# Optimization experiments

Hardware: AMD Instinct MI355X
Metric: run time of the kernel (lower is better)

The kernel has to match this reference:

```python
import jax, jax.numpy as jnp
import numpy as np

P_DROP = 0.2
NEG_SLOPE = 0.2


def setup_inputs() -> dict:
    key = jax.random.key(0)
    ks = jax.random.split(key, 12)
    N, E = 50000, 800000
    IN, H1, H2, OUT = 256, 256, 128, 64
    x = jax.random.normal(ks[0], (N, IN), dtype=jnp.float32)
    adj_rows = jax.random.randint(ks[1], (E,), 0, N, dtype=jnp.int32)
    adj_cols = jax.random.randint(ks[2], (E,), 0, N, dtype=jnp.int32)
    adj_vals = jax.random.uniform(ks[3], (E,), dtype=jnp.float32)
    W1 = jax.random.normal(ks[4], (H1, IN), dtype=jnp.float32) * (1.0 / np.sqrt(IN))
    b1 = jax.random.normal(ks[5], (H1,), dtype=jnp.float32) * 0.01
    W2 = jax.random.normal(ks[6], (H2, H1), dtype=jnp.float32) * (1.0 / np.sqrt(H1))
    b2 = jax.random.normal(ks[7], (H2,), dtype=jnp.float32) * 0.01
    W3 = jax.random.normal(ks[8], (OUT, H2), dtype=jnp.float32) * (1.0 / np.sqrt(H2))
    b3 = jax.random.normal(ks[9], (OUT,), dtype=jnp.float32) * 0.01
    mask1 = jax.random.bernoulli(ks[10], 1.0 - P_DROP, (N, H1))
    mask2 = jax.random.bernoulli(ks[11], 1.0 - P_DROP, (N, H2))
    return {"x": x, "adj_rows": adj_rows, "adj_cols": adj_cols, "adj_vals": adj_vals,
            "W1": W1, "b1": b1, "W2": W2, "b2": b2, "W3": W3, "b3": b3,
            "mask1": mask1, "mask2": mask2}


def _spmm(rows, cols, vals, h, n_nodes):
    # sparse adjacency matmul: out[r] = sum_e vals[e] * h[cols[e]] for rows[e]==r
    msgs = vals[:, None] * h[cols]  # [E, d] irregular gather
    return jax.ops.segment_sum(msgs, rows, num_segments=n_nodes)


def _gcn_layer(x, W, b, rows, cols, vals, n_nodes):
    h = x @ W.T + b  # nn.Linear
    return _spmm(rows, cols, vals, h, n_nodes)


def reference(x, adj_rows, adj_cols, adj_vals, W1, b1, W2, b2, W3, b3, mask1, mask2):
    N = x.shape[0]
    keep = 1.0 / (1.0 - P_DROP)
    h = _gcn_layer(x, W1, b1, adj_rows, adj_cols, adj_vals, N)
    h = jnp.where(h >= 0, h, NEG_SLOPE * h)
    h = jnp.where(mask1, h * keep, 0.0)
    h = _gcn_layer(h, W2, b2, adj_rows, adj_cols, adj_vals, N)
    h = jnp.where(h >= 0, h, NEG_SLOPE * h)
    h = jnp.where(mask2, h * keep, 0.0)
    z = _gcn_layer(h, W3, b3, adj_rows, adj_cols, adj_vals, N)
    return z
```

## Files before the change

kernel.cpp:

```cpp
#include <hip/hip_runtime.h>


typedef unsigned short ushort_t;
typedef __attribute__((ext_vector_type(8))) short bf16x8;
typedef __attribute__((ext_vector_type(4))) float f32x4;
typedef __attribute__((ext_vector_type(2))) unsigned int u32x2;
typedef __attribute__((ext_vector_type(4))) unsigned int u32x4;

__device__ __forceinline__ float bf2f(ushort_t u) {
  return __uint_as_float(((unsigned int)u) << 16);
}
__device__ __forceinline__ ushort_t f2bf(float f) {
  unsigned int u = __float_as_uint(f);
  return (ushort_t)((u + 0x7FFFu + ((u >> 16) & 1u)) >> 16);
}
__device__ __forceinline__ float read_f(const void* p, int fm, size_t i) {
  return fm ? bf2f(((const ushort_t*)p)[i]) : ((const float*)p)[i];
}

__device__ __forceinline__ size_t frag_off(int m, int k, int K) {
  return (size_t)(m >> 4) * 16 * K + ((size_t)(k >> 5) << 9) +
         (((k >> 3) & 3) << 7) + ((m & 15) << 3) + (k & 7);
}

__global__ void prep_kernel(const void* __restrict__ x,
                            const void* __restrict__ m1,
                            const void* __restrict__ m2,
                            int* __restrict__ modes,
                            int* __restrict__ zero_region, int zn,
                            const void* __restrict__ W1, const void* __restrict__ W2,
                            const void* __restrict__ W3,
                            const void* __restrict__ b1, const void* __restrict__ b2,
                            const void* __restrict__ b3,
                            ushort_t* __restrict__ whi, ushort_t* __restrict__ wlo,
                            float* __restrict__ biasf,
                            int n1, int n2, int n3, int h1, int h2, int h3,
                            int K1, int K2, int K3) {
  if (blockIdx.x == 0) {
    __shared__ int bfok;
    if (threadIdx.x == 0) bfok = 1;
    __syncthreads();
    for (int i = threadIdx.x; i < 8192; i += blockDim.x) {
      ushort_t h = ((const ushort_t*)x)[i];
      int e = (h >> 7) & 0xFF;
      if (!(h == 0 || (e >= 95 && e <= 133))) atomicAnd(&bfok, 0);
    }
    __syncthreads();
    if (threadIdx.x == 0) modes[0] = bfok;
  } else if (blockIdx.x <= 2) {
    const void* p = (blockIdx.x == 1) ? m1 : m2;
    __shared__ int ok[4];
    if (threadIdx.x < 4) ok[threadIdx.x] = 1;
    __syncthreads();
    for (int i = threadIdx.x; i < 4096; i += blockDim.x) {
      unsigned int w = ((const unsigned int*)p)[i];
      if (!(w == 0u || w == 1u)) atomicAnd(&ok[0], 0);
      if (!(w == 0u || w == 0x3F800000u)) atomicAnd(&ok[1], 0);
      unsigned int h16 = w >> 16, l16 = w & 0xFFFFu;
      if (!((h16 == 0u || h16 == 0x3F80u) && (l16 == 0u || l16 == 0x3F80u)))
        atomicAnd(&ok[2], 0);
      if (((w | (w >> 8) | (w >> 16) | (w >> 24)) & 0xFEu) != 0u) atomicAnd(&ok[3], 0);
    }
    __syncthreads();
    if (threadIdx.x == 0)
      modes[blockIdx.x] = ok[0] ? 1 : (ok[1] ? 2 : (ok[2] ? 3 : 0));
  } else if (blockIdx.x < 35) {
    __shared__ int bfok;
    if (threadIdx.x == 0) bfok = 1;
    __syncthreads();
    for (int i = threadIdx.x; i < 8192; i += blockDim.x) {
      ushort_t h = ((const ushort_t*)x)[i];
      int e = (h >> 7) & 0xFF;
      if (!(h == 0 || (e >= 95 && e <= 133))) atomicAnd(&bfok, 0);
    }
    __syncthreads();
    int fm = bfok;
    int wtot = n1 + n2 + n3;
    int total = wtot + h1 + h2 + h3;
    for (int i = (blockIdx.x - 3) * 256 + threadIdx.x; i < total; i += 32 * 256) {
      if (i < wtot) {
        const void* src; int j, K; size_t base;
        if (i < n1) { src = W1; j = i; K = K1; base = 0; }
        else if (i < n1 + n2) { src = W2; j = i - n1; K = K2; base = n1; }
        else { src = W3; j = i - n1 - n2; K = K3; base = (size_t)n1 + n2; }
        int n = j / K, k = j - n * K;
        float v = read_f(src, fm, j);
        ushort_t h = f2bf(v);
        size_t o = base + frag_off(n, k, K);
        whi[o] = h;
        wlo[o] = f2bf(v - bf2f(h));
      } else {
        int k = i - wtot;
        const void* src; int j;
        if (k < h1) { src = b1; j = k; }
        else if (k < h1 + h2) { src = b2; j = k - h1; }
        else { src = b3; j = k - h1 - h2; }
        biasf[k] = read_f(src, fm, j);
      }
    }
  } else {
    int i = (blockIdx.x - 35) * blockDim.x + threadIdx.x;
    int stride = (gridDim.x - 35) * blockDim.x;
    for (; i < zn; i += stride) zero_region[i] = 0;
  }
}

__global__ void hist_bin_kernel(
    const int* __restrict__ rows, const int* __restrict__ cols,
    const void* __restrict__ vals, const int* __restrict__ fm_p,
    int* __restrict__ h8, int* __restrict__ cnt_ovf, int* __restrict__ binfill,
    int2* __restrict__ bins, int cap, int use_bins, int4* __restrict__ ovf,
    int E, int Nrows, const void* __restrict__ x, ushort_t* __restrict__ xbf,
    int K1, int nx) {
  int fm = *fm_p;
  const int BIN_BLOCKS = 1024;
  if (blockIdx.x < BIN_BLOCKS) {
    int xcd = blockIdx.x & 7;
    if (use_bins) {
      __shared__ int hist[8];
      __shared__ int gbase[8];
      __shared__ int pfx[8];
      __shared__ int2 stage[1024];
      int tid = threadIdx.x;
      for (int tb = blockIdx.x; tb * 1024 < E; tb += BIN_BLOCKS) {
        int base = tb * 1024;
        if (tid < 8) hist[tid] = 0;
        __syncthreads();
        int rr[4], cc[4], pp[4], rk[4]; float vv[4];
#pragma unroll
        for (int j = 0; j < 4; ++j) {
          int i = base + j * 256 + tid;
          if (i < E) {
            rr[j] = rows[i]; cc[j] = cols[i]; vv[j] = read_f(vals, fm, i);
            pp[j] = rr[j] >> 13;
            rk[j] = atomicAdd(&hist[pp[j]], 1);
          } else {
            pp[j] = -1;
          }
        }
        __syncthreads();
        if (tid == 0) {
          int s = 0;
#pragma unroll
          for (int q = 0; q < 8; ++q) { pfx[q] = s; s += hist[q]; }
        }
        if (tid < 8)
          gbase[tid] = atomicAdd(&binfill[(xcd << 4) + tid], hist[tid]);
        __syncthreads();
#pragma unroll
        for (int j = 0; j < 4; ++j) {
          if (pp[j] >= 0)
            stage[pfx[pp[j]] + rk[j]] =
                make_int2((rr[j] << 16) | cc[j], __float_as_int(vv[j]));
        }
        __syncthreads();
        int total = pfx[7] + hist[7];
        for (int k = tid; k < total; k += 256) {
          int p = 0;
#pragma unroll
          for (int q = 1; q < 8; ++q) p += (k >= pfx[q]);
          int2 ent = stage[k];
          int pos = gbase[p] + (k - pfx[p]);
          if (pos < cap) {
            bins[(size_t)((xcd << 3) + p) * cap + pos] = ent;
          } else {
            int r = ((unsigned int)ent.x) >> 16;
            int orank = atomicAdd(&cnt_ovf[r], 1);
            int op = atomicAdd(&binfill[128], 1);
            ovf[op] = make_int4(r, ent.x & 0xFFFF, ent.y, orank);
          }
        }
        __syncthreads();
      }
    } else {
      int* cnt_s = h8 + (size_t)xcd * Nrows;
      int i = blockIdx.x * blockDim.x + threadIdx.x;
      int stride = BIN_BLOCKS * blockDim.x;
      for (; i < E; i += stride) atomicAdd(&cnt_s[rows[i]], 1);
    }
  } else {
    if (fm == 1) return;
    int nx4 = nx / 4;
    int i = (blockIdx.x - BIN_BLOCKS) * blockDim.x + threadIdx.x;
    int stride = (gridDim.x - BIN_BLOCKS) * blockDim.x;
    for (; i < nx4; i += stride) {
      int m = i / (K1 / 4);
      int k0 = (i - m * (K1 / 4)) * 4;
      f32x4 v = ((const f32x4*)x)[i];
      ushort_t p0 = f2bf(v[0]), p1 = f2bf(v[1]), p2 = f2bf(v[2]), p3 = f2bf(v[3]);
      size_t o = frag_off(m, k0, K1);
      *(u32x2*)(xbf + o) = (u32x2){
          (unsigned int)p0 | ((unsigned int)p1 << 16),
          (unsigned int)p2 | ((unsigned int)p3 << 16)};
    }
  }
}

__global__ __launch_bounds__(256) void count_kernel(
    const int2* __restrict__ bins, const int* __restrict__ binfill,
    int cap, int* __restrict__ h8, int Nrows, int use_bins) {
  if (!use_bins) return;
  int x = blockIdx.x >> 3, p = blockIdx.x & 7;
  __shared__ int hist[8192];
  for (int i = threadIdx.x; i < 8192; i += 256) hist[i] = 0;
  __syncthreads();
  int n = binfill[x * 16 + p];
  if (n > cap) n = cap;
  const int2* bp = bins + (size_t)((x << 3) + p) * cap;
  for (int e = threadIdx.x; e < n; e += 256) {
    int r = ((unsigned int)bp[e].x) >> 16;
    atomicAdd(&hist[r & 8191], 1);
  }
  __syncthreads();
  int r0 = p << 13;
  for (int i = threadIdx.x; i < 8192; i += 256) {
    int r = r0 + i;
    if (r < Nrows) h8[(size_t)x * Nrows + r] = hist[i];
  }
}

__global__ __launch_bounds__(256) void scan_fused_kernel(
    const int* __restrict__ h8, const int* __restrict__ cnt_ovf,
    int* __restrict__ pub, int* __restrict__ row_start,
    int* __restrict__ sb8, int n) {
  int b = blockIdx.x, t = threadIdx.x;
  int i = b * 256 + t;
  int hx[8];
  int v = 0, ov = 0;
  if (i < n) {
#pragma unroll
    for (int x = 0; x < 8; ++x) { hx[x] = h8[(size_t)x * n + i]; v += hx[x]; }
    ov = cnt_ovf[i];
  } else {
#pragma unroll
    for (int x = 0; x < 8; ++x) hx[x] = 0;
  }
  int vt = v + ov;
  __shared__ int s[256];
  s[t] = vt;
  __syncthreads();
  for (int off = 1; off < 256; off <<= 1) {
    int a_ = s[t];
    int y_ = (t >= off) ? s[t - off] : 0;
    __syncthreads();
    s[t] = a_ + y_;
    __syncthreads();
  }
  int incl = s[t];
  int total = s[255];
  if (t == 0)
    __hip_atomic_store(&pub[b], (total << 1) | 1, __ATOMIC_RELEASE,
                       __HIP_MEMORY_SCOPE_AGENT);
  int contrib = 0;
  for (int t0 = t; t0 < b; t0 += 256) {
    int p;
    do {
      p = __hip_atomic_load(&pub[t0], __ATOMIC_ACQUIRE,
                            __HIP_MEMORY_SCOPE_AGENT);
    } while (!(p & 1));
    contrib += (p >> 1);
  }
  __syncthreads();
  s[t] = contrib;
  __syncthreads();
  for (int off = 128; off > 0; off >>= 1) {
    if (t < off) s[t] += s[t + off];
    __syncthreads();
  }
  int base = s[0];
  int rs = base + incl - vt;
  if (i < n) {
    row_start[i] = rs;
    int acc = rs;
#pragma unroll
    for (int x = 0; x < 8; ++x) { sb8[(size_t)x * n + i] = acc; acc += hx[x]; }
    sb8[(size_t)8 * n + i] = acc;
  }
  if (i == n - 1) row_start[n] = base + incl;
}

template<int KC>
__device__ __forceinline__ void load_afrag(const ushort_t* __restrict__ A,
                                           const ushort_t* __restrict__ Xrow,
                                           bool rowA, int mtile, int K,
                                           int lane, int mr, int quad, int M,
                                           bf16x8* dst) {
  if (rowA) {
    int rr = mtile * 16 + mr;
    if (rr >= M) rr = M - 1;
    const ushort_t* ap = Xrow + (size_t)rr * K + quad * 8;
#pragma unroll
    for (int kc = 0; kc < KC; ++kc) dst[kc] = *(const bf16x8*)(ap + kc * 32);
  } else {
    const ushort_t* ap = A + (size_t)mtile * 16 * K + lane * 8;
#pragma unroll
    for (int kc = 0; kc < KC; ++kc) dst[kc] = *(const bf16x8*)(ap + kc * 512);
  }
}

template<int KC>
__device__ __forceinline__ void gemm_dev(
    int vbid, int nblk, int tid,
    const ushort_t* __restrict__ A, const ushort_t* __restrict__ Xrow, int fm,
    const ushort_t* __restrict__ Whi, const ushort_t* __restrict__ Wlo,
    const float* __restrict__ bias, ushort_t* __restrict__ g, int ldg,
    int M, int nct) {
  const int K = KC * 32;
  int wave = tid >> 6, lane = tid & 63;
  int gw = vbid * 4 + wave;
  int NW = nblk * 4;
  int mr = lane & 15, quad = lane >> 4;
  int ct = gw % nct;
  int nrt = (M + 15) >> 4;
  int ntasks = nct * nrt;
  if (gw >= ntasks) return;

  bool rowA = (Xrow != nullptr) && (fm != 0);

  bf16x8 wh[KC], wl[KC];
  {
    const ushort_t* wp = Whi + (size_t)ct * 16 * K + lane * 8;
    const ushort_t* wq = Wlo + (size_t)ct * 16 * K + lane * 8;
#pragma unroll
    for (int kc = 0; kc < KC; ++kc) {
      wh[kc] = *(const bf16x8*)(wp + kc * 512);
      wl[kc] = *(const bf16x8*)(wq + kc * 512);
    }
  }
  int col = ct * 16 + mr;
  float bv = bias[col];

  int task = gw;
  bf16x8 af[KC];
  load_afrag<KC>(A, Xrow, rowA, task / nct, K, lane, mr, quad, M, af);

#pragma unroll 1
  for (;;) {
    int next = task + NW;
    bool has_next = next < ntasks;
    bf16x8 afn[KC];
    if (has_next)
      load_afrag<KC>(A, Xrow, rowA, next / nct, K, lane, mr, quad, M, afn);

    f32x4 acc[4];
#pragma unroll
    for (int t = 0; t < 4; ++t) acc[t] = (f32x4){0.f, 0.f, 0.f, 0.f};
#pragma unroll
    for (int kc = 0; kc < KC; ++kc) {
      acc[(2 * kc) & 3] = __builtin_amdgcn_mfma_f32_16x16x32_bf16(af[kc], wh[kc], acc[(2 * kc) & 3], 0, 0, 0);
      acc[(2 * kc + 1) & 3] = __builtin_amdgcn_mfma_f32_16x16x32_bf16(af[kc], wl[kc], acc[(2 * kc + 1) & 3], 0, 0, 0);
    }
    int m0 = (task / nct) * 16;
#pragma unroll
    for (int r = 0; r < 4; ++r) {
      int row = m0 + quad * 4 + r;
      float s = ((acc[0][r] + acc[1][r]) + (acc[2][r] + acc[3][r])) + bv;
      if (row < M) g[(size_t)row * ldg + col] = f2bf(s);
    }
    if (!has_next) break;
#pragma unroll
    for (int kc = 0; kc < KC; ++kc) af[kc] = afn[kc];
    task = next;
  }
}

template<int KC>
__global__ __launch_bounds__(256) void gemm_breg_kernel(
    const ushort_t* __restrict__ A,
    const ushort_t* __restrict__ Xrow, const int* __restrict__ fm_p,
    const ushort_t* __restrict__ Whi, const ushort_t* __restrict__ Wlo,
    const float* __restrict__ bias, ushort_t* __restrict__ g, int ldg,
    int M, int nct) {
  gemm_dev<KC>(blockIdx.x, gridDim.x, threadIdx.x, A, Xrow, *fm_p,
               Whi, Wlo, bias, g, ldg, M, nct);
}

__global__ __launch_bounds__(256) void scatter_gemm_kernel(
    const int2* __restrict__ bins, const int* __restrict__ binfill,
    const int* __restrict__ row_start, int* __restrict__ fill,
    const int* __restrict__ sb8, int Nrows,
    int2* __restrict__ ecv, int cap, const int4* __restrict__ ovf,
    const int* __restrict__ rows, const int* __restrict__ cols,
    const void* __restrict__ vals, const int* __restrict__ fm_p,
    int use_bins, int E,
    const ushort_t* __restrict__ A, const ushort_t* __restrict__ Xrow,
    const ushort_t* __restrict__ Whi, const ushort_t* __restrict__ Wlo,
    const float* __restrict__ bias, ushort_t* __restrict__ g, int ldg,
    int M, int nct) {
  __shared__ int sbl[8192];
  if (blockIdx.x >= 64) {
    gemm_dev<8>(blockIdx.x - 64, 1024, threadIdx.x, A, Xrow, *fm_p,
                Whi, Wlo, bias, g, ldg, M, nct);
    return;
  }
  if (use_bins) {
    int x = blockIdx.x >> 3, p = blockIdx.x & 7;
    int r0 = p << 13;
    for (int i = threadIdx.x; i < 8192; i += 256) {
      int r = r0 + i;
      sbl[i] = (r < Nrows) ? sb8[(size_t)x * Nrows + r] : 0;
    }
    __syncthreads();
    int n = binfill[x * 16 + p];
    if (n > cap) n = cap;
    const int2* bp = bins + (size_t)((x << 3) + p) * cap;
    for (int e = threadIdx.x; e < n; e += 256) {
      int2 ent = bp[e];
      int r = ((unsigned int)ent.x) >> 16;
      int pos = atomicAdd(&sbl[r & 8191], 1);
      ecv[pos] = make_int2(ent.x & 0xFFFF, ent.y);
    }
    int ovfn = binfill[128];
    for (int e = blockIdx.x * 256 + (int)threadIdx.x; e < ovfn; e += 64 * 256) {
      int4 t = ovf[e];
      ecv[sb8[(size_t)8 * Nrows + t.x] + t.w] = make_int2(t.y, t.z);
    }
  } else {
    int fm = *fm_p;
    for (int i = blockIdx.x * 256 + (int)threadIdx.x; i < E; i += 64 * 256) {
      int r = rows[i];
      int pos = atomicAdd(&fill[r], 1);
      ecv[row_start[r] + pos] = make_int2(cols[i], __float_as_int(read_f(vals, fm, i)));
    }
  }
}

template<int VEC, int CHUNK, bool CLAMP>
__device__ __forceinline__ void spmm_chunk(const int2* __restrict__ ecv,
                                           int base, int e1,
                                           const ushort_t* __restrict__ G,
                                           int D, int f0, float* a) {
  int2 cv[CHUNK];
#pragma unroll
  for (int j = 0; j < CHUNK; ++j) {
    int ee = base + j;
    if (CLAMP) ee = (ee < e1) ? ee : e1 - 1;
    cv[j] = ecv[ee];
  }
  float v[CHUNK];
#pragma unroll
  for (int j = 0; j < CHUNK; ++j) {
    v[j] = __int_as_float(cv[j].y);
    if (CLAMP && (base + j >= e1)) v[j] = 0.f;
  }
  if (VEC == 4) {
    u32x2 gg[CHUNK];
#pragma unroll
    for (int j = 0; j < CHUNK; ++j)
      gg[j] = *(const u32x2*)(G + (size_t)cv[j].x * D + f0);
#pragma unroll
    for (int j = 0; j < CHUNK; ++j) {
      a[0] += v[j] * bf2f((ushort_t)gg[j][0]);
      a[1] += v[j] * bf2f((ushort_t)(gg[j][0] >> 16));
      a[2] += v[j] * bf2f((ushort_t)gg[j][1]);
      a[3] += v[j] * bf2f((ushort_t)(gg[j][1] >> 16));
    }
  } else if (VEC == 2) {
    unsigned int gg[CHUNK];
#pragma unroll
    for (int j = 0; j < CHUNK; ++j)
      gg[j] = *(const unsigned int*)(G + (size_t)cv[j].x * D + f0);
#pragma unroll
    for (int j = 0; j < CHUNK; ++j) {
      a[0] += v[j] * bf2f((ushort_t)gg[j]);
      a[1] += v[j] * bf2f((ushort_t)(gg[j] >> 16));
    }
  } else {
    ushort_t h[CHUNK];
#pragma unroll
    for (int j = 0; j < CHUNK; ++j) h[j] = G[(size_t)cv[j].x * D + f0];
#pragma unroll
    for (int j = 0; j < CHUNK; ++j) a[0] += v[j] * bf2f(h[j]);
  }
}

template<int MODE, int VEC>
__global__ __launch_bounds__(256) void spmm8_kernel(
    const int* __restrict__ row_start, const int2* __restrict__ ecv,
    const ushort_t* __restrict__ G, int D,
    const void* __restrict__ mask, const int* __restrict__ mmode_p,
    void* __restrict__ outp, int N) {
  __shared__ ushort_t stage[1024];
  int wave = threadIdx.x >> 6, lane = threadIdx.x & 63;
  int r = blockIdx.x * 4 + wave;
  bool active = r < N;
  float a[VEC];
#pragma unroll
  for (int q = 0; q < VEC; ++q) a[q] = 0.f;
  int f0 = lane * VEC;

  bool keep[VEC];
#pragma unroll
  for (int q = 0; q < VEC; ++q) keep[q] = true;
  if (MODE == 1 && active) {
    size_t om = (size_t)r * D + f0;
    int mm = *mmode_p;
    if (mm == 1 || mm == 2) {
      if (VEC == 4) {
        u32x4 mv = *(const u32x4*)((const unsigned int*)mask + om);
#pragma unroll
        for (int q = 0; q < VEC; ++q) keep[q] = mv[q] != 0u;
      } else if (VEC == 2) {
        u32x2 mv = *(const u32x2*)((const unsigned int*)mask + om);
#pragma unroll
        for (int q = 0; q < VEC; ++q) keep[q] = mv[q] != 0u;
      } else {
        keep[0] = ((const unsigned int*)mask)[om] != 0u;
      }
    } else if (mm == 3) {
      if (VEC == 4) {
        u32x2 mv = *(const u32x2*)((const ushort_t*)mask + om);
        keep[0] = (mv[0] & 0xFFFFu) != 0u; keep[1] = (mv[0] >> 16) != 0u;
        keep[2] = (mv[1] & 0xFFFFu) != 0u; keep[3] = (mv[1] >> 16) != 0u;
      } else if (VEC == 2) {
        unsigned int mv = *(const unsigned int*)((const ushort_t*)mask + om);
        keep[0] = (mv & 0xFFFFu) != 0u; keep[1] = (mv >> 16) != 0u;
      } else {
        keep[0] = ((const ushort_t*)mask)[om] != 0;
      }
    } else {
      if (VEC == 4) {
        unsigned int mv = *(const unsigned int*)((const unsigned char*)mask + om);
        keep[0] = (mv & 0xFFu) != 0u;         keep[1] = ((mv >> 8) & 0xFFu) != 0u;
        keep[2] = ((mv >> 16) & 0xFFu) != 0u; keep[3] = (mv >> 24) != 0u;
      } else if (VEC == 2) {
        unsigned int mv = *(const unsigned short*)((const unsigned char*)mask + om);
        keep[0] = (mv & 0xFFu) != 0u; keep[1] = ((mv >> 8) & 0xFFu) != 0u;
      } else {
        keep[0] = ((const unsigned char*)mask)[om] != 0;
      }
    }
  }

  if (active) {
    int e  = __builtin_amdgcn_readfirstlane(row_start[r]);
    int e1 = __builtin_amdgcn_readfirstlane(row_start[r + 1]);
    for (; e + 16 <= e1; e += 16)
      spmm_chunk<VEC, 16, false>(ecv, e, e1, G, D, f0, a);
    for (; e < e1; e += 8)
      spmm_chunk<VEC, 8, true>(ecv, e, e1, G, D, f0, a);
  }

  if (MODE == 1) {
    if (active) {
#pragma unroll
      for (int q = 0; q < VEC; ++q) {
        float t = a[q];
        t = (t >= 0.f) ? t : 0.2f * t;
        t = keep[q] ? t * 1.25f : 0.f;
        stage[wave * D + f0 + q] = f2bf(t);
      }
    }
    __syncthreads();
    if (threadIdx.x < D) {
      int g = threadIdx.x >> 3, s = threadIdx.x & 7;
      int kc = g >> 2, quad = g & 3;
      int sr = s >> 1;
      int r0 = blockIdx.x * 4;
      if (r0 + sr < N) {
        int kk = kc * 32 + quad * 8 + (s & 1) * 4;
        size_t dst = (size_t)(r0 >> 4) * 16 * D + ((size_t)kc << 9) +
                     (quad << 7) + ((r0 & 15) << 3) + s * 4;
        *(u32x2*)((ushort_t*)outp + dst) = *(const u32x2*)(stage + sr * D + kk);
      }
    }
  } else {
    if (active) {
      size_t o = (size_t)r * D + f0;
#pragma unroll
      for (int q = 0; q < VEC; ++q) ((float*)outp)[o + q] = a[q];
    }
  }
}

extern "C" void kernel_launch(void* const* d_in, const int* in_sizes, int n_in,
                              void* d_out, int out_size, void* d_ws, size_t ws_size,
                              hipStream_t stream) {
  const void* x     = d_in[0];
  const int*  rows  = (const int*)d_in[1];
  const int*  cols  = (const int*)d_in[2];
  const void* vals  = d_in[3];
  const void* W1    = d_in[4];
  const void* b1    = d_in[5];
  const void* W2    = d_in[6];
  const void* b2    = d_in[7];
  const void* W3    = d_in[8];
  const void* b3    = d_in[9];
  const void* mask1 = d_in[10];
  const void* mask2 = d_in[11];

  const int H1  = in_sizes[5];
  const int H2  = in_sizes[7];
  const int OUT = in_sizes[9];
  const int IN  = in_sizes[4] / H1;
  const int N   = in_sizes[0] / IN;
  const int E   = in_sizes[1];
  const int W1n = in_sizes[4], W2n = in_sizes[6], W3n = in_sizes[8];
  const int Np  = ((N + 15) / 16) * 16;
  const int CAP = (E >> 5) + 2048;
  const int use_bins = (N <= 65535) ? 1 : 0;
  const int P = (N + 255) / 256;

  char* ws = (char*)d_ws;
  size_t off = 0;
  auto alloc = [&](size_t bytes) -> void* {
    void* p = ws + off;
    off = (off + bytes + 255) & ~(size_t)255;
    return p;
  };
  int*      modes     = (int*)alloc(4 * 4);
  int*      row_start = (int*)alloc((size_t)(N + 1) * 4);
  int*      meta      = (int*)alloc(((size_t)10 * N + 512) * 4);
  int*      sb8       = (int*)alloc((size_t)9 * N * 4);
  int2*     ecv       = (int2*)alloc((size_t)E * 8);
  int2*     bins      = (int2*)alloc((size_t)64 * CAP * 8);
  int4*     ovf       = (int4*)alloc((size_t)E * 16);
  ushort_t* whi       = (ushort_t*)alloc((size_t)(W1n + W2n + W3n) * 2);
  ushort_t* wlo       = (ushort_t*)alloc((size_t)(W1n + W2n + W3n) * 2);
  float*    biasf     = (float*)alloc((size_t)(H1 + H2 + OUT) * 4);
  ushort_t* bufA      = (ushort_t*)alloc((size_t)Np * H1 * 2);
  ushort_t* bufB      = (ushort_t*)alloc((size_t)Np * H1 * 2);
  ushort_t* bufC      = (ushort_t*)bins;

  int* fmode   = modes;
  int* mm1     = modes + 1;
  int* mm2     = modes + 2;
  int* h8      = meta;
  int* cnt_ovf = meta + 8 * N;
  int* fill    = meta + 9 * N;
  int* binfill = meta + 10 * N;
  int* pub     = meta + 10 * N + 256;
  ushort_t* w1hi = whi,             *w1lo = wlo;
  ushort_t* w2hi = whi + W1n,       *w2lo = wlo + W1n;
  ushort_t* w3hi = whi + W1n + W2n, *w3lo = wlo + W1n + W2n;

  prep_kernel<<<512, 256, 0, stream>>>(
      x, mask1, mask2, modes, meta, 10 * N + 512,
      W1, W2, W3, b1, b2, b3, whi, wlo, biasf,
      W1n, W2n, W3n, H1, H2, OUT, IN, H1, H2);

  hist_bin_kernel<<<2048, 256, 0, stream>>>(
      rows, cols, vals, fmode, h8, cnt_ovf, binfill, bins, CAP, use_bins, ovf,
      E, N, x, bufA, IN, N * IN);

  count_kernel<<<64, 256, 0, stream>>>(bins, binfill, CAP, h8, N, use_bins);

  scan_fused_kernel<<<P, 256, 0, stream>>>(h8, cnt_ovf, pub, row_start, sb8, N);

  scatter_gemm_kernel<<<1088, 256, 0, stream>>>(
      bins, binfill, row_start, fill, sb8, N, ecv, CAP, ovf,
      rows, cols, vals, fmode, use_bins, E,
      bufA, (const ushort_t*)x, w1hi, w1lo, biasf, bufB, H1, N, H1 / 16);

  int spmm_grid = (N + 3) / 4;
  const int GEMM_BLOCKS = 1024;

  spmm8_kernel<1, 4><<<spmm_grid, 256, 0, stream>>>(
      row_start, ecv, bufB, H1, mask1, mm1, bufC, N);
  gemm_breg_kernel<8><<<GEMM_BLOCKS, 256, 0, stream>>>(
      bufC, nullptr, fmode, w2hi, w2lo, biasf + H1, bufB, H2, N, H2 / 16);
  spmm8_kernel<1, 2><<<spmm_grid, 256, 0, stream>>>(
      row_start, ecv, bufB, H2, mask2, mm2, bufA, N);
  gemm_breg_kernel<4><<<GEMM_BLOCKS, 256, 0, stream>>>(
      bufA, nullptr, fmode, w3hi, w3lo, biasf + H1 + H2, bufB, OUT, N, OUT / 16);
  spmm8_kernel<0, 1><<<spmm_grid, 256, 0, stream>>>(
      row_start, ecv, bufB, OUT, nullptr, fmode, d_out, N);
}
```

Baseline: 406.7 us.

## Store GEMM outputs in 32-column panels and run SpMM per panel

```diff
diff --git a/kernel.cpp b/kernel.cpp
--- a/kernel.cpp
+++ b/kernel.cpp
@@ -303,7 +303,7 @@
     int vbid, int nblk, int tid,
     const ushort_t* __restrict__ A, const ushort_t* __restrict__ Xrow, int fm,
     const ushort_t* __restrict__ Whi, const ushort_t* __restrict__ Wlo,
-    const float* __restrict__ bias, ushort_t* __restrict__ g, int ldg,
+    const float* __restrict__ bias, ushort_t* __restrict__ g, int Np,
     int M, int nct) {
   const int K = KC * 32;
   int wave = tid >> 6, lane = tid & 63;
@@ -329,6 +329,7 @@
   }
   int col = ct * 16 + mr;
   float bv = bias[col];
+  ushort_t* gp = g + (size_t)(col >> 5) * Np * 32 + (col & 31);
 
   int task = gw;
   bf16x8 af[KC];
@@ -355,7 +356,7 @@
     for (int r = 0; r < 4; ++r) {
       int row = m0 + quad * 4 + r;
       float s = ((acc[0][r] + acc[1][r]) + (acc[2][r] + acc[3][r])) + bv;
-      if (row < M) g[(size_t)row * ldg + col] = f2bf(s);
+      if (row < M) gp[(size_t)row * 32] = f2bf(s);
     }
     if (!has_next) break;
 #pragma unroll
@@ -369,10 +370,10 @@
     const ushort_t* __restrict__ A,
     const ushort_t* __restrict__ Xrow, const int* __restrict__ fm_p,
     const ushort_t* __restrict__ Whi, const ushort_t* __restrict__ Wlo,
-    const float* __restrict__ bias, ushort_t* __restrict__ g, int ldg,
+    const float* __restrict__ bias, ushort_t* __restrict__ g, int Np,
     int M, int nct) {
   gemm_dev<KC>(blockIdx.x, gridDim.x, threadIdx.x, A, Xrow, *fm_p,
-               Whi, Wlo, bias, g, ldg, M, nct);
+               Whi, Wlo, bias, g, Np, M, nct);
 }
 
 __global__ __launch_bounds__(256) void scatter_gemm_kernel(
@@ -385,12 +386,12 @@
     int use_bins, int E,
     const ushort_t* __restrict__ A, const ushort_t* __restrict__ Xrow,
     const ushort_t* __restrict__ Whi, const ushort_t* __restrict__ Wlo,
-    const float* __restrict__ bias, ushort_t* __restrict__ g, int ldg,
+    const float* __restrict__ bias, ushort_t* __restrict__ g, int Np,
     int M, int nct) {
   __shared__ int sbl[8192];
   if (blockIdx.x >= 64) {
     gemm_dev<8>(blockIdx.x - 64, 1024, threadIdx.x, A, Xrow, *fm_p,
-                Whi, Wlo, bias, g, ldg, M, nct);
+                Whi, Wlo, bias, g, Np, M, nct);
     return;
   }
   if (use_bins) {
@@ -425,151 +426,79 @@
   }
 }
 
-template<int VEC, int CHUNK, bool CLAMP>
-__device__ __forceinline__ void spmm_chunk(const int2* __restrict__ ecv,
-                                           int base, int e1,
-                                           const ushort_t* __restrict__ G,
-                                           int D, int f0, float* a) {
-  int2 cv[CHUNK];
-#pragma unroll
-  for (int j = 0; j < CHUNK; ++j) {
-    int ee = base + j;
-    if (CLAMP) ee = (ee < e1) ? ee : e1 - 1;
-    cv[j] = ecv[ee];
-  }
-  float v[CHUNK];
-#pragma unroll
-  for (int j = 0; j < CHUNK; ++j) {
-    v[j] = __int_as_float(cv[j].y);
-    if (CLAMP && (base + j >= e1)) v[j] = 0.f;
-  }
-  if (VEC == 4) {
-    u32x2 gg[CHUNK];
-#pragma unroll
-    for (int j = 0; j < CHUNK; ++j)
-      gg[j] = *(const u32x2*)(G + (size_t)cv[j].x * D + f0);
-#pragma unroll
-    for (int j = 0; j < CHUNK; ++j) {
-      a[0] += v[j] * bf2f((ushort_t)gg[j][0]);
-      a[1] += v[j] * bf2f((ushort_t)(gg[j][0] >> 16));
-      a[2] += v[j] * bf2f((ushort_t)gg[j][1]);
-      a[3] += v[j] * bf2f((ushort_t)(gg[j][1] >> 16));
-    }
-  } else if (VEC == 2) {
-    unsigned int gg[CHUNK];
-#pragma unroll
-    for (int j = 0; j < CHUNK; ++j)
-      gg[j] = *(const unsigned int*)(G + (size_t)cv[j].x * D + f0);
-#pragma unroll
-    for (int j = 0; j < CHUNK; ++j) {
-      a[0] += v[j] * bf2f((ushort_t)gg[j]);
-      a[1] += v[j] * bf2f((ushort_t)(gg[j] >> 16));
+template<int MODE>
+__global__ __launch_bounds__(256) void spmmp_kernel(
+    const int* __restrict__ row_start, const int2* __restrict__ ecv,
+    const ushort_t* __restrict__ Gp, int D, int Np,
+    const void* __restrict__ mask, const int* __restrict__ mmode_p,
+    void* __restrict__ outp, int N, int npanel) {
+  __shared__ ushort_t stage[256];
+  int p = blockIdx.x % npanel;
+  int rg = blockIdx.x / npanel;
+  int wave = threadIdx.x >> 6, lane = threadIdx.x & 63;
+  int half = lane >> 5, f = lane & 31;
+  int r = rg * 8 + wave * 2 + half;
+  bool active = r < N;
+  const ushort_t* G0 = Gp + (size_t)p * Np * 32;
+  float a = 0.f;
+
+  bool keep = true;
+  if (MODE == 1 && active) {
+    size_t om = (size_t)r * D + p * 32 + f;
+    int mm = *mmode_p;
+    if (mm == 1 || mm == 2) keep = ((const unsigned int*)mask)[om] != 0u;
+    else if (mm == 3)       keep = ((const ushort_t*)mask)[om] != 0;
+    else                    keep = ((const unsigned char*)mask)[om] != 0;
+  }
+
+  if (active) {
+    int e = row_start[r], e1 = row_start[r + 1];
+    for (; e + 8 <= e1; e += 8) {
+      int2 cv[8];
+#pragma unroll
+      for (int j = 0; j < 8; ++j) cv[j] = ecv[e + j];
+      ushort_t g[8];
+#pragma unroll
+      for (int j = 0; j < 8; ++j) g[j] = G0[(size_t)cv[j].x * 32 + f];
+#pragma unroll
+      for (int j = 0; j < 8; ++j) a += __int_as_float(cv[j].y) * bf2f(g[j]);
+    }
+    if (e < e1) {
+      int idx[8]; float v[8];
+#pragma unroll
+      for (int j = 0; j < 8; ++j) {
+        int ee = e + j;
+        bool ok = ee < e1;
+        int2 cv = ecv[ok ? ee : e1 - 1];
+        idx[j] = cv.x;
+        v[j] = ok ? __int_as_float(cv.y) : 0.f;
+      }
+      ushort_t g[8];
+#pragma unroll
+      for (int j = 0; j < 8; ++j) g[j] = G0[(size_t)idx[j] * 32 + f];
+#pragma unroll
+      for (int j = 0; j < 8; ++j) a += v[j] * bf2f(g[j]);
+    }
+  }
+
+  if (MODE == 1) {
+    float t = (a >= 0.f) ? a : 0.2f * a;
+    t = keep ? t * 1.25f : 0.f;
+    stage[threadIdx.x] = active ? f2bf(t) : (ushort_t)0;
+    __syncthreads();
+    if (threadIdx.x < 64) {
+      int k = threadIdx.x;
+      int quad = k >> 4, idx = k & 15;
+      int row = idx >> 1, s = (idx & 1) * 4;
+      int r0 = rg * 8;
+      size_t base = (size_t)(r0 >> 4) * 16 * D + ((size_t)p << 9) +
+                    (size_t)(r0 & 15) * 8;
+      size_t goff = base + quad * 128 + idx * 4;
+      *(u32x2*)((ushort_t*)outp + goff) =
+          *(const u32x2*)(stage + row * 32 + quad * 8 + s);
     }
   } else {
-    ushort_t h[CHUNK];
-#pragma unroll
-    for (int j = 0; j < CHUNK; ++j) h[j] = G[(size_t)cv[j].x * D + f0];
-#pragma unroll
-    for (int j = 0; j < CHUNK; ++j) a[0] += v[j] * bf2f(h[j]);
-  }
-}
-
-template<int MODE, int VEC>
-__global__ __launch_bounds__(256) void spmm8_kernel(
-    const int* __restrict__ row_start, const int2* __restrict__ ecv,
-    const ushort_t* __restrict__ G, int D,
-    const void* __restrict__ mask, const int* __restrict__ mmode_p,
-    void* __restrict__ outp, int N) {
-  __shared__ ushort_t stage[1024];
-  int wave = threadIdx.x >> 6, lane = threadIdx.x & 63;
-  int r = blockIdx.x * 4 + wave;
-  bool active = r < N;
-  float a[VEC];
-#pragma unroll
-  for (int q = 0; q < VEC; ++q) a[q] = 0.f;
-  int f0 = lane * VEC;
-
-  bool keep[VEC];
-#pragma unroll
-  for (int q = 0; q < VEC; ++q) keep[q] = true;
-  if (MODE == 1 && active) {
-    size_t om = (size_t)r * D + f0;
-    int mm = *mmode_p;
-    if (mm == 1 || mm == 2) {
-      if (VEC == 4) {
-        u32x4 mv = *(const u32x4*)((const unsigned int*)mask + om);
-#pragma unroll
-        for (int q = 0; q < VEC; ++q) keep[q] = mv[q] != 0u;
-      } else if (VEC == 2) {
-        u32x2 mv = *(const u32x2*)((const unsigned int*)mask + om);
-#pragma unroll
-        for (int q = 0; q < VEC; ++q) keep[q] = mv[q] != 0u;
-      } else {
-        keep[0] = ((const unsigned int*)mask)[om] != 0u;
-      }
-    } else if (mm == 3) {
-      if (VEC == 4) {
-        u32x2 mv = *(const u32x2*)((const ushort_t*)mask + om);
-        keep[0] = (mv[0] & 0xFFFFu) != 0u; keep[1] = (mv[0] >> 16) != 0u;
-        keep[2] = (mv[1] & 0xFFFFu) != 0u; keep[3] = (mv[1] >> 16) != 0u;
-      } else if (VEC == 2) {
-        unsigned int mv = *(const unsigned int*)((const ushort_t*)mask + om);
-        keep[0] = (mv & 0xFFFFu) != 0u; keep[1] = (mv >> 16) != 0u;
-      } else {
-        keep[0] = ((const ushort_t*)mask)[om] != 0;
-      }
-    } else {
-      if (VEC == 4) {
-        unsigned int mv = *(const unsigned int*)((const unsigned char*)mask + om);
-        keep[0] = (mv & 0xFFu) != 0u;         keep[1] = ((mv >> 8) & 0xFFu) != 0u;
-        keep[2] = ((mv >> 16) & 0xFFu) != 0u; keep[3] = (mv >> 24) != 0u;
-      } else if (VEC == 2) {
-        unsigned int mv = *(const unsigned short*)((const unsigned char*)mask + om);
-        keep[0] = (mv & 0xFFu) != 0u; keep[1] = ((mv >> 8) & 0xFFu) != 0u;
-      } else {
-        keep[0] = ((const unsigned char*)mask)[om] != 0;
-      }
-    }
-  }
-
-  if (active) {
-    int e  = __builtin_amdgcn_readfirstlane(row_start[r]);
-    int e1 = __builtin_amdgcn_readfirstlane(row_start[r + 1]);
-    for (; e + 16 <= e1; e += 16)
-      spmm_chunk<VEC, 16, false>(ecv, e, e1, G, D, f0, a);
-    for (; e < e1; e += 8)
-      spmm_chunk<VEC, 8, true>(ecv, e, e1, G, D, f0, a);
-  }
-
-  if (MODE == 1) {
-    if (active) {
-#pragma unroll
-      for (int q = 0; q < VEC; ++q) {
-        float t = a[q];
-        t = (t >= 0.f) ? t : 0.2f * t;
-        t = keep[q] ? t * 1.25f : 0.f;
-        stage[wave * D + f0 + q] = f2bf(t);
-      }
-    }
-    __syncthreads();
-    if (threadIdx.x < D) {
-      int g = threadIdx.x >> 3, s = threadIdx.x & 7;
-      int kc = g >> 2, quad = g & 3;
-      int sr = s >> 1;
-      int r0 = blockIdx.x * 4;
-      if (r0 + sr < N) {
-        int kk = kc * 32 + quad * 8 + (s & 1) * 4;
-        size_t dst = (size_t)(r0 >> 4) * 16 * D + ((size_t)kc << 9) +
-                     (quad << 7) + ((r0 & 15) << 3) + s * 4;
-        *(u32x2*)((ushort_t*)outp + dst) = *(const u32x2*)(stage + sr * D + kk);
-      }
-    }
-  } else {
-    if (active) {
-      size_t o = (size_t)r * D + f0;
-#pragma unroll
-      for (int q = 0; q < VEC; ++q) ((float*)outp)[o + q] = a[q];
-    }
+    if (active) ((float*)outp)[(size_t)r * D + p * 32 + f] = a;
   }
 }
 
@@ -650,19 +579,19 @@
   scatter_gemm_kernel<<<1088, 256, 0, stream>>>(
       bins, binfill, row_start, fill, sb8, N, ecv, CAP, ovf,
       rows, cols, vals, fmode, use_bins, E,
-      bufA, (const ushort_t*)x, w1hi, w1lo, biasf, bufB, H1, N, H1 / 16);
-
-  int spmm_grid = (N + 3) / 4;
+      bufA, (const ushort_t*)x, w1hi, w1lo, biasf, bufB, Np, N, H1 / 16);
+
+  const int RGB = (N + 7) / 8;
   const int GEMM_BLOCKS = 1024;
 
-  spmm8_kernel<1, 4><<<spmm_grid, 256, 0, stream>>>(
-      row_start, ecv, bufB, H1, mask1, mm1, bufC, N);
+  spmmp_kernel<1><<<8 * RGB, 256, 0, stream>>>(
+      row_start, ecv, bufB, H1, Np, mask1, mm1, bufC, N, 8);
   gemm_breg_kernel<8><<<GEMM_BLOCKS, 256, 0, stream>>>(
-      bufC, nullptr, fmode, w2hi, w2lo, biasf + H1, bufB, H2, N, H2 / 16);
-  spmm8_kernel<1, 2><<<spmm_grid, 256, 0, stream>>>(
-      row_start, ecv, bufB, H2, mask2, mm2, bufA, N);
+      bufC, nullptr, fmode, w2hi, w2lo, biasf + H1, bufB, Np, N, H2 / 16);
+  spmmp_kernel<1><<<4 * RGB, 256, 0, stream>>>(
+      row_start, ecv, bufB, H2, Np, mask2, mm2, bufA, N, 4);
   gemm_breg_kernel<4><<<GEMM_BLOCKS, 256, 0, stream>>>(
-      bufA, nullptr, fmode, w3hi, w3lo, biasf + H1 + H2, bufB, OUT, N, OUT / 16);
-  spmm8_kernel<0, 1><<<spmm_grid, 256, 0, stream>>>(
-      row_start, ecv, bufB, OUT, nullptr, fmode, d_out, N);
-}
+      bufA, nullptr, fmode, w3hi, w3lo, biasf + H1 + H2, bufB, Np, N, OUT / 16);
+  spmmp_kernel<0><<<2 * RGB, 256, 0, stream>>>(
+      row_start, ecv, bufB, OUT, Np, nullptr, fmode, d_out, N, 2);
+}
```

New measurement: 548.0 us. +34.7%, slower.
